# Kernel tuning notes

Measured on AMD Instinct MI355X. Metric: run time of the kernel, lower is better.

The kernel has to match this reference:

```python
import jax, jax.numpy as jnp
import numpy as np

# CustomConvLayer with a 3x3-tap .kof file, global defaults:
#   operation: x * w, input_encode: x, kernel_encode: w
# => out[b,o,h,w] = sum_c sum_k x_pad[b,c,h+dh_k,w+dw_k] * weights[o,c,k]
# Tap offsets: integer stencil (dh,dw) in {0,1,2}^2 (k_elems=9), padding=1, stride=1.

PAD = 1
TAPS = [(dh, dw) for dh in range(3) for dw in range(3)]  # 9 taps


def setup_inputs() -> dict:
    key = jax.random.key(0)
    k1, k2 = jax.random.split(key)
    x = jax.random.normal(k1, (16, 64, 128, 128), dtype=jnp.float32)
    # learned per-tap weights: [out_channels, in_channels, k_elems]
    weights = jax.random.normal(k2, (128, 64, 9), dtype=jnp.float32) * 0.05
    return {"x": x, "weights": weights}


def reference(x, weights):
    B, C, H, Wd = x.shape
    xp = jnp.pad(x, ((0, 0), (0, 0), (PAD, PAD), (PAD, PAD)))
    # gather per-tap shifted views: [B, C, K, H, W]
    gathered = jnp.stack([xp[:, :, dh:dh + H, dw:dw + Wd] for dh, dw in TAPS], axis=2)
    # per-tap op x*w, then combine over in_channels and taps
    out = jnp.einsum('bckhw,ock->bohw', gathered, weights)
    return out
```

## Files before the change

kernel.cpp:

```cpp
#include <hip/hip_runtime.h>
#include <hip/hip_bf16.h>
#include <stdint.h>


typedef __bf16 bf16x8 __attribute__((ext_vector_type(8)));
typedef float  f32x4  __attribute__((ext_vector_type(4)));

__global__ __launch_bounds__(256) void xform_w(const float* __restrict__ wgt,
                                               __bf16* __restrict__ BtF) {
  const int t = blockIdx.x * 256 + threadIdx.x;
  if (t >= 9216) return;
  const int s = t >> 9, rem = t & 511, quad = rem >> 7, n = rem & 127;
  bf16x8 o;
#pragma unroll
  for (int r = 0; r < 8; ++r) {
    const int k = s * 32 + quad * 8 + r;
    const int tap = k >> 6, c = k & 63;
    o[r] = (__bf16)wgt[(n * 64 + c) * 9 + tap];
  }
  *(bf16x8*)(BtF + (size_t)t * 8) = o;
}

__global__ __launch_bounds__(256) void conv_mfma(const float* __restrict__ x,
                                                 const __bf16* __restrict__ BtF,
                                                 float* __restrict__ out) {
  __shared__ alignas(16) __bf16 Aslab[3120 * 8];
  __shared__ alignas(16) __bf16 T[2][64][40];
  const int tid  = threadIdx.x;
  const int lane = tid & 63;
  const int wave = tid >> 6;
  const int quad = lane >> 4;
  const int l16  = lane & 15;
  const int rank = (blockIdx.x & 7) * 256 + (blockIdx.x >> 3);
  const int b = rank >> 7;
  const int h = rank & 127;
  const int wm = wave >> 1;
  const int wn = wave & 1;

  if (tid < 48) {
    const int r3 = tid >> 4, wp = ((tid >> 3) & 1) * 129, cq = tid & 7;
    const int v = r3 * 130 + wp;
    const bf16x8 z = {};
    *(bf16x8*)(Aslab + (size_t)(v * 8 + (cq ^ (v & 7))) * 8) = z;
  }

  const int cS   = tid >> 2;
  const int wS   = (tid & 3) * 8;
  const int wloc = tid & 31;
  const int cqG  = tid >> 5;
  const float* xc = x + ((size_t)b * 64 + cS) * 16384;

  f32x4 g[3][2];

#define XR_OF(u) (h - 1 + ((u) >> 2))
#define ISSUE(u) do {                                                         \
    const int xr_  = XR_OF(u);                                                \
    const int xrc_ = xr_ < 0 ? 0 : (xr_ > 127 ? 127 : xr_);                   \
    const float* p_ = xc + (size_t)xrc_ * 128 + ((u) & 3) * 32 + wS;          \
    g[(u) % 3][0] = *(const f32x4*)p_;                                        \
    g[(u) % 3][1] = *(const f32x4*)(p_ + 4);                                  \
  } while (0)

  ISSUE(0);
  ISSUE(1);
#pragma unroll
  for (int u = 0; u < 12; ++u) {
    if (u < 10) ISSUE(u + 2);
    {
      const int xr_ = XR_OF(u);
      f32x4 a0 = g[u % 3][0], a1 = g[u % 3][1];
      if (xr_ < 0 || xr_ > 127) { a0 = (f32x4){}; a1 = (f32x4){}; }
      bf16x8 pk;
      pk[0] = (__bf16)a0[0]; pk[1] = (__bf16)a0[1];
      pk[2] = (__bf16)a0[2]; pk[3] = (__bf16)a0[3];
      pk[4] = (__bf16)a1[0]; pk[5] = (__bf16)a1[1];
      pk[6] = (__bf16)a1[2]; pk[7] = (__bf16)a1[3];
      *(bf16x8*)&T[u & 1][cS][wS] = pk;
    }
    asm volatile("s_waitcnt lgkmcnt(0)" ::: "memory");
    __builtin_amdgcn_s_barrier();
    __builtin_amdgcn_sched_barrier(0);
    {
      bf16x8 o;
#pragma unroll
      for (int j = 0; j < 8; ++j) o[j] = T[u & 1][cqG * 8 + j][wloc];
      const int v = (u >> 2) * 130 + ((u & 3) << 5) + wloc + 1;
      *(bf16x8*)(Aslab + (size_t)(v * 8 + (cqG ^ (v & 7))) * 8) = o;
    }
  }
  asm volatile("s_waitcnt lgkmcnt(0)" ::: "memory");
  __builtin_amdgcn_s_barrier();
  __builtin_amdgcn_sched_barrier(0);

  f32x4 acc[4][4] = {};
#pragma unroll
  for (int s = 0; s < 18; ++s) {
    const int tap = s >> 1;
    const int dh = tap / 3, dw = tap % 3;
    const int cq = ((s & 1) << 2) + quad;
    bf16x8 aF[4], bF[4];
#pragma unroll
    for (int i = 0; i < 4; ++i) {
      const int m = (wm << 6) + (i << 4) + l16;
      const int v = dh * 130 + m + dw;
      const int slot = (v << 3) + (cq ^ (v & 7));
      aF[i] = *(const bf16x8*)(Aslab + (size_t)slot * 8);
      const int n = (wn << 6) + (i << 4) + l16;
      bF[i] = *(const bf16x8*)(BtF + ((size_t)((s * 4 + quad) * 128 + n) << 3));
    }
#pragma unroll
    for (int i = 0; i < 4; ++i)
#pragma unroll
      for (int j = 0; j < 4; ++j)
        acc[i][j] = __builtin_amdgcn_mfma_f32_16x16x32_bf16(aF[i], bF[j], acc[i][j], 0, 0, 0);
  }

#pragma unroll
  for (int j = 0; j < 4; ++j) {
    const int n = (wn << 6) + (j << 4) + l16;
    float* orow = out + (((size_t)(b * 128 + n) * 128 + h) << 7);
#pragma unroll
    for (int i = 0; i < 4; ++i) {
      const int m0 = (wm << 6) + (i << 4) + (quad << 2);
      __builtin_nontemporal_store(acc[i][j], (f32x4*)(orow + m0));
    }
  }
}

__global__ void conv_naive(const float* __restrict__ x, const float* __restrict__ wgt,
                           float* __restrict__ out, int total) {
  int idx = blockIdx.x * 256 + threadIdx.x;
  if (idx >= total) return;
  const int w = idx & 127;
  const int h = (idx >> 7) & 127;
  const int o = (idx >> 14) & 127;
  const int b = idx >> 21;
  float s = 0.f;
  for (int c = 0; c < 64; ++c) {
    const float* xc = x + ((size_t)(b * 64 + c) * 128) * 128;
    const float* wc = wgt + (o * 64 + c) * 9;
    for (int dh = 0; dh < 3; ++dh) {
      const int hh = h + dh - 1;
      if (hh < 0 || hh >= 128) continue;
      for (int dw = 0; dw < 3; ++dw) {
        const int ww = w + dw - 1;
        if (ww < 0 || ww >= 128) continue;
        s += xc[hh * 128 + ww] * wc[dh * 3 + dw];
      }
    }
  }
  out[idx] = s;
}

extern "C" void kernel_launch(void* const* d_in, const int* in_sizes, int n_in,
                              void* d_out, int out_size, void* d_ws, size_t ws_size,
                              hipStream_t stream) {
  const float* x   = (const float*)d_in[0];
  const float* wgt = (const float*)d_in[1];
  float* out = (float*)d_out;

  const size_t BTF_BYTES = 9216ull * 16;

  if (ws_size < BTF_BYTES) {
    const int total = 16 * 128 * 128 * 128;
    conv_naive<<<(total + 255) / 256, 256, 0, stream>>>(x, wgt, out, total);
    return;
  }

  __bf16* BtF = (__bf16*)d_ws;

  xform_w<<<36, 256, 0, stream>>>(wgt, BtF);
  conv_mfma<<<2048, 256, 0, stream>>>(x, BtF, out);
}
```

Measured before the change: 230.8 us.

## Load input channel-strided to skip LDS transpose and per-step barriers

Each thread now reads 8 channels of one column with scalar strided loads (coalesced across the 32 threads that share a channel group) and packs them straight into the swizzled A slab. This removes the staging transpose buffer and the 12 barriers in the prologue, leaving one __syncthreads before the MFMA loop. A 4-deep register prefetch replaces the 3-deep vector prefetch, at the cost of more scalar global load instructions. Output stores also switch from nontemporal to regular stores.

```diff
diff --git a/kernel.cpp b/kernel.cpp
--- a/kernel.cpp
+++ b/kernel.cpp
@@ -25,7 +25,6 @@
                                                  const __bf16* __restrict__ BtF,
                                                  float* __restrict__ out) {
   __shared__ alignas(16) __bf16 Aslab[3120 * 8];
-  __shared__ alignas(16) __bf16 T[2][64][40];
   const int tid  = threadIdx.x;
   const int lane = tid & 63;
   const int wave = tid >> 6;
@@ -44,53 +43,41 @@
     *(bf16x8*)(Aslab + (size_t)(v * 8 + (cq ^ (v & 7))) * 8) = z;
   }
 
-  const int cS   = tid >> 2;
-  const int wS   = (tid & 3) * 8;
-  const int wloc = tid & 31;
-  const int cqG  = tid >> 5;
-  const float* xc = x + ((size_t)b * 64 + cS) * 16384;
+  const int c8 = tid >> 5;
+  const int wl = tid & 31;
+  const float* xb = x + ((size_t)b * 64 + c8 * 8) * 16384 + wl;
 
-  f32x4 g[3][2];
+  float f[4][8];
 
-#define XR_OF(u) (h - 1 + ((u) >> 2))
-#define ISSUE(u) do {                                                         \
-    const int xr_  = XR_OF(u);                                                \
-    const int xrc_ = xr_ < 0 ? 0 : (xr_ > 127 ? 127 : xr_);                   \
-    const float* p_ = xc + (size_t)xrc_ * 128 + ((u) & 3) * 32 + wS;          \
-    g[(u) % 3][0] = *(const f32x4*)p_;                                        \
-    g[(u) % 3][1] = *(const f32x4*)(p_ + 4);                                  \
+#define T_ISSUE(T) do {                                                       \
+    const int u_ = (T) >> 2, p_ = (T) & 3;                                    \
+    const int xr_ = h - 1 + u_;                                               \
+    if (xr_ >= 0 && xr_ <= 127) {                                             \
+      const float* p0_ = xb + (size_t)xr_ * 128 + p_ * 32;                    \
+      _Pragma("unroll")                                                       \
+      for (int cc = 0; cc < 8; ++cc) f[(T) & 3][cc] = p0_[(size_t)cc * 16384];\
+    }                                                                         \
   } while (0)
 
-  ISSUE(0);
-  ISSUE(1);
+#define T_CONSUME(T) do {                                                     \
+    const int u_ = (T) >> 2, p_ = (T) & 3;                                    \
+    const int xr_ = h - 1 + u_;                                               \
+    bf16x8 pk = {};                                                           \
+    if (xr_ >= 0 && xr_ <= 127) {                                             \
+      _Pragma("unroll")                                                       \
+      for (int cc = 0; cc < 8; ++cc) pk[cc] = (__bf16)f[(T) & 3][cc];         \
+    }                                                                         \
+    const int v_ = u_ * 130 + 1 + p_ * 32 + wl;                               \
+    *(bf16x8*)(Aslab + (size_t)(v_ * 8 + (c8 ^ (v_ & 7))) * 8) = pk;          \
+  } while (0)
+
+  T_ISSUE(0); T_ISSUE(1); T_ISSUE(2);
 #pragma unroll
-  for (int u = 0; u < 12; ++u) {
-    if (u < 10) ISSUE(u + 2);
-    {
-      const int xr_ = XR_OF(u);
-      f32x4 a0 = g[u % 3][0], a1 = g[u % 3][1];
-      if (xr_ < 0 || xr_ > 127) { a0 = (f32x4){}; a1 = (f32x4){}; }
-      bf16x8 pk;
-      pk[0] = (__bf16)a0[0]; pk[1] = (__bf16)a0[1];
-      pk[2] = (__bf16)a0[2]; pk[3] = (__bf16)a0[3];
-      pk[4] = (__bf16)a1[0]; pk[5] = (__bf16)a1[1];
-      pk[6] = (__bf16)a1[2]; pk[7] = (__bf16)a1[3];
-      *(bf16x8*)&T[u & 1][cS][wS] = pk;
-    }
-    asm volatile("s_waitcnt lgkmcnt(0)" ::: "memory");
-    __builtin_amdgcn_s_barrier();
-    __builtin_amdgcn_sched_barrier(0);
-    {
-      bf16x8 o;
-#pragma unroll
-      for (int j = 0; j < 8; ++j) o[j] = T[u & 1][cqG * 8 + j][wloc];
-      const int v = (u >> 2) * 130 + ((u & 3) << 5) + wloc + 1;
-      *(bf16x8*)(Aslab + (size_t)(v * 8 + (cqG ^ (v & 7))) * 8) = o;
-    }
+  for (int t = 0; t < 12; ++t) {
+    if (t < 9) T_ISSUE(t + 3);
+    T_CONSUME(t);
   }
-  asm volatile("s_waitcnt lgkmcnt(0)" ::: "memory");
-  __builtin_amdgcn_s_barrier();
-  __builtin_amdgcn_sched_barrier(0);
+  __syncthreads();
 
   f32x4 acc[4][4] = {};
 #pragma unroll
@@ -122,7 +109,7 @@
 #pragma unroll
     for (int i = 0; i < 4; ++i) {
       const int m0 = (wm << 6) + (i << 4) + (quad << 2);
-      __builtin_nontemporal_store(acc[i][j], (f32x4*)(orow + m0));
+      *(f32x4*)(orow + m0) = acc[i][j];
     }
   }
 }
```

After: 219.6 us. 4.9% less time.
